# Kernel tuning notes

Hardware: AMD Instinct MI355X
Metric: run time of the kernel (lower is better)

Reference implementation:

```python
import jax, jax.numpy as jnp
import numpy as np

H = 16  # num heads
D = 64  # head dim


def rotate_half(x):
    h = x.shape[-1] // 2
    return jnp.concatenate([-x[..., h:], x[..., :h]], axis=-1)


def setup_inputs() -> dict:
    key = jax.random.key(0)
    ks = jax.random.split(key, 8)
    B, S, E = 2, 4096, 1024
    scale = 1.0 / np.sqrt(E)
    x = jax.random.normal(ks[0], (B, S, E), dtype=jnp.float32)
    Wq = jax.random.normal(ks[1], (E, E), dtype=jnp.float32) * scale
    Wk = jax.random.normal(ks[2], (E, E), dtype=jnp.float32) * scale
    Wv = jax.random.normal(ks[3], (E, E), dtype=jnp.float32) * scale
    Wg = jax.random.normal(ks[4], (E, E), dtype=jnp.float32) * scale
    Wo = jax.random.normal(ks[5], (E, E), dtype=jnp.float32) * scale
    cos = jax.random.normal(ks[6], (S, D), dtype=jnp.float32)
    sin = jax.random.normal(ks[7], (S, D), dtype=jnp.float32)
    return {"x": x, "Wq": Wq, "Wk": Wk, "Wv": Wv, "Wg": Wg, "Wo": Wo,
            "cos": cos, "sin": sin, "block_size": 256}


def reference(x, Wq, Wk, Wv, Wg, Wo, cos, sin, block_size):
    B, S, E = x.shape
    nb = S // block_size  # seq divisible by block_size (remainder==0 path)

    gate = (x @ Wg).reshape(B, S, H, D)
    q = (x @ Wq).reshape(B, S, H, D)
    k = (x @ Wk).reshape(B, S, H, D)
    v = (x @ Wv).reshape(B, S, H, D)

    # RoPE: cos/sin [S, D] -> broadcast over batch and heads (unsqueeze_dim=1 in torch
    # with [S, 1, D] after slicing gives the same broadcast over the head axis here).
    c = cos[:S][None, :, None, :]  # [1, S, 1, D]
    s = sin[:S][None, :, None, :]
    q = q * c + rotate_half(q) * s
    k = k * c + rotate_half(k) * s

    # Block-diagonal attention: reshape seq into blocks and attend within blocks only.
    def to_blocks(t):  # [B,S,H,D] -> [B,nb,H,block,D]
        return t.reshape(B, nb, block_size, H, D).transpose(0, 1, 3, 2, 4)

    qb, kb, vb = to_blocks(q), to_blocks(k), to_blocks(v)
    scores = jnp.einsum('bnhqd,bnhkd->bnhqk', qb, kb) / np.sqrt(D)
    attn = jax.nn.softmax(scores, axis=-1)
    ob = jnp.einsum('bnhqk,bnhkd->bnhqd', attn, vb)

    out = ob.transpose(0, 1, 3, 2, 4).reshape(B, S, H, D)  # back to [B,S,H,D]
    out = (out * jax.nn.sigmoid(gate)).reshape(B, S, H * D)
    return out @ Wo
```

## Files before the change

### kernel.cpp

```cpp
#include <hip/hip_runtime.h>
#include <hip/hip_bf16.h>
#include <stdint.h>

typedef __bf16 bf16_t;
typedef __bf16 bf16x8 __attribute__((ext_vector_type(8)));
typedef float f32x4 __attribute__((ext_vector_type(4)));

#define DEVI __device__ __forceinline__

constexpr int BB = 2;
constexpr int SS = 4096;
constexpr int EE = 1024;
constexpr int HH = 16;
constexpr int DD = 64;
constexpr int MM = BB * SS;

DEVI void gload16(const void* g, void* l) {
  __builtin_amdgcn_global_load_lds(
      (const __attribute__((address_space(1))) void*)g,
      (__attribute__((address_space(3))) void*)l, 16, 0, 0);
}

__global__ void cvt_kernel(const float* __restrict__ in, bf16_t* __restrict__ out, int n8) {
  int i = blockIdx.x * 256 + threadIdx.x;
  if (i >= n8) return;
  const float* p = in + (size_t)i * 8;
  bf16x8 o;
#pragma unroll
  for (int j = 0; j < 8; ++j) o[j] = (bf16_t)p[j];
  *(bf16x8*)(out + (size_t)i * 8) = o;
}

__global__ void wt_kernel(const float* __restrict__ w0, const float* __restrict__ w1,
                          const float* __restrict__ w2, const float* __restrict__ w3,
                          const float* __restrict__ w4, bf16_t* __restrict__ out) {
  __shared__ float tile[32][33];
  const float* Wsel = blockIdx.z == 0 ? w0 : blockIdx.z == 1 ? w1 :
                      blockIdx.z == 2 ? w2 : blockIdx.z == 3 ? w3 : w4;
  bf16_t* O = out + (size_t)blockIdx.z * EE * EE;
  int n0 = blockIdx.x * 32, k0 = blockIdx.y * 32;
  int tx = threadIdx.x & 31, ty = threadIdx.x >> 5;
#pragma unroll
  for (int i = 0; i < 4; ++i)
    tile[ty + i * 8][tx] = Wsel[(size_t)(k0 + ty + i * 8) * EE + n0 + tx];
  __syncthreads();
#pragma unroll
  for (int i = 0; i < 4; ++i)
    O[(size_t)(n0 + ty + i * 8) * EE + k0 + tx] = (bf16_t)tile[tx][ty + i * 8];
}

__global__ __launch_bounds__(512, 2) void gemm8p(const bf16_t* __restrict__ A,
                                                 const bf16_t* __restrict__ Bt,
                                                 bf16_t* __restrict__ Obase,
                                                 const float* __restrict__ cosp,
                                                 const float* __restrict__ sinp) {
  __shared__ bf16_t Al[2][2][128][64];
  __shared__ bf16_t Bl[2][2][128][64];
  const int id = blockIdx.x;
  const int swz = (id & 7) * 64 + (id >> 3);
  const int bx = swz >> 4, by = swz & 15;
  const int m0 = bx << 8, n0 = by << 8;
  const int tid = threadIdx.x, wv = tid >> 6, ln = tid & 63;
  const int wm = wv >> 2, wn = wv & 3;
  const int sr = tid >> 3;
  const int scs = (tid & 7) ^ (sr & 7);
  const bf16_t* Abase = A + ((size_t)(m0 + sr) << 10) + scs * 8;
  const bf16_t* Bbase = Bt + ((size_t)(n0 + sr) << 10) + scs * 8;

  f32x4 acc[8][4] = {};
  bf16x8 bfr[4][2];

#define STA(BUFI, H, J, KT) \
  gload16(Abase + (((H)*128 + (J)*64) << 10) + (KT)*64, &Al[BUFI][H][(J)*64 + wv * 8][0])
#define STB(BUFI, H, J, KT) \
  gload16(Bbase + (((H)*128 + (J)*64) << 10) + (KT)*64, &Bl[BUFI][H][(J)*64 + wv * 8][0])
#define STB_ALL(BUFI, KT) do { STB(BUFI,0,0,KT); STB(BUFI,0,1,KT); STB(BUFI,1,0,KT); STB(BUFI,1,1,KT); } while (0)

#define PHASE(BUFI, MH, KK, LDB, STAGEC, WAITC) do {                           \
    bf16x8 af_[4];                                                             \
    _Pragma("unroll") for (int mi_ = 0; mi_ < 4; ++mi_) {                      \
      int ar_ = (MH)*64 + mi_*16 + (ln & 15);                                  \
      int ach_ = ((KK)*4 + (ln >> 4)) ^ (ar_ & 7);                             \
      af_[mi_] = *(const bf16x8*)&Al[BUFI][wm][ar_][ach_ * 8];                 \
    }                                                                          \
    if (LDB) {                                                                 \
      _Pragma("unroll") for (int ni_ = 0; ni_ < 4; ++ni_) {                    \
        int br_ = (wn & 1)*64 + ni_*16 + (ln & 15);                            \
        int bch_ = ((KK)*4 + (ln >> 4)) ^ (br_ & 7);                           \
        bfr[ni_][KK] = *(const bf16x8*)&Bl[BUFI][wn >> 1][br_][bch_ * 8];      \
      }                                                                        \
    }                                                                          \
    STAGEC;                                                                    \
    WAITC;                                                                     \
    __builtin_amdgcn_s_barrier();                                              \
    asm volatile("s_waitcnt lgkmcnt(0)" ::: "memory");                         \
    __builtin_amdgcn_sched_barrier(0);                                         \
    __builtin_amdgcn_s_setprio(1);                                             \
    _Pragma("unroll") for (int mi_ = 0; mi_ < 4; ++mi_)                        \
      _Pragma("unroll") for (int ni_ = 0; ni_ < 4; ++ni_)                      \
        acc[(MH)*4 + mi_][ni_] = __builtin_amdgcn_mfma_f32_16x16x32_bf16(      \
            af_[mi_], bfr[ni_][KK], acc[(MH)*4 + mi_][ni_], 0, 0, 0);          \
    __builtin_amdgcn_s_setprio(0);                                             \
    __builtin_amdgcn_s_barrier();                                              \
    asm volatile("" ::: "memory");                                             \
  } while (0)

  STA(0, 0, 0, 0); STA(0, 1, 0, 0);
  STB_ALL(0, 0);
  STA(0, 0, 1, 0); STA(0, 1, 1, 0);
  STA(1, 0, 0, 1); STA(1, 1, 0, 1);
  STB_ALL(1, 1);
  asm volatile("s_waitcnt vmcnt(6)" ::: "memory");
  __builtin_amdgcn_s_barrier();
  asm volatile("" ::: "memory");

#pragma unroll 1
  for (int i = 0; i < 7; ++i) {
    const int to = 2 * i + 1;
    PHASE(0, 0, 0, 1, ({ STA(1, 0, 1, to); STA(1, 1, 1, to); }), ((void)0));
    PHASE(0, 0, 1, 1, ((void)0), ((void)0));
    PHASE(0, 1, 0, 0, ({ STA(0, 0, 0, to + 1); STA(0, 1, 0, to + 1); STB_ALL(0, to + 1); }),
          ((void)0));
    PHASE(0, 1, 1, 0, ((void)0), ({ asm volatile("s_waitcnt vmcnt(6)" ::: "memory"); }));
    PHASE(1, 0, 0, 1, ({ STA(0, 0, 1, to + 1); STA(0, 1, 1, to + 1); }), ((void)0));
    PHASE(1, 0, 1, 1, ((void)0), ((void)0));
    PHASE(1, 1, 0, 0, ({ STA(1, 0, 0, to + 2); STA(1, 1, 0, to + 2); STB_ALL(1, to + 2); }),
          ((void)0));
    PHASE(1, 1, 1, 0, ((void)0), ({ asm volatile("s_waitcnt vmcnt(6)" ::: "memory"); }));
  }
  PHASE(0, 0, 0, 1, ({ STA(1, 0, 1, 15); STA(1, 1, 1, 15); }), ((void)0));
  PHASE(0, 0, 1, 1, ((void)0), ((void)0));
  PHASE(0, 1, 0, 0, ((void)0), ((void)0));
  PHASE(0, 1, 1, 0, ((void)0), ({ asm volatile("s_waitcnt vmcnt(0)" ::: "memory"); }));
  PHASE(1, 0, 0, 1, ((void)0), ((void)0));
  PHASE(1, 0, 1, 1, ((void)0), ((void)0));
  PHASE(1, 1, 0, 0, ((void)0), ((void)0));
  PHASE(1, 1, 1, 0, ((void)0), ((void)0));
#undef PHASE
#undef STA
#undef STB
#undef STB_ALL

  const int widx = n0 >> 10;
  const int cb = (n0 & 1023) + wn * 64;
  bf16_t* W = Obase + (size_t)widx * MM * EE;
  if (widx <= 1) {
#pragma unroll
    for (int mi = 0; mi < 8; ++mi) {
#pragma unroll
      for (int r = 0; r < 4; ++r) {
        int row = m0 + wm * 128 + mi * 16 + ((ln >> 4) << 2) + r;
        int s = row & (SS - 1);
        float cv[4], sv[4];
#pragma unroll
        for (int ni = 0; ni < 4; ++ni) {
          int d = ni * 16 + (ln & 15);
          cv[ni] = cosp[s * DD + d];
          sv[ni] = sinp[s * DD + d];
        }
#pragma unroll
        for (int ni = 0; ni < 4; ++ni) {
          float v = acc[mi][ni][r], p = acc[mi][ni ^ 2][r];
          float o = v * cv[ni] + (ni < 2 ? -p : p) * sv[ni];
          W[(size_t)row * EE + cb + ni * 16 + (ln & 15)] = (bf16_t)o;
        }
      }
    }
  } else if (widx == 2) {
#pragma unroll
    for (int mi = 0; mi < 8; ++mi)
#pragma unroll
      for (int ni = 0; ni < 4; ++ni) {
        int row = m0 + wm * 128 + mi * 16 + ((ln >> 4) << 2);
        int ncol = cb + ni * 16 + (ln & 15);
        int h = ncol >> 6, d = ncol & 63;
        int b = row >> 12, s = row & (SS - 1);
        bf16_t* p = W + (((size_t)b * HH + h) * DD + d) * SS + s;
#pragma unroll
        for (int r = 0; r < 4; ++r) p[r] = (bf16_t)acc[mi][ni][r];
      }
  } else {
#pragma unroll
    for (int mi = 0; mi < 8; ++mi)
#pragma unroll
      for (int ni = 0; ni < 4; ++ni) {
        int row = m0 + wm * 128 + mi * 16 + ((ln >> 4) << 2);
        int ncol = cb + ni * 16 + (ln & 15);
        bf16_t* p = W + (size_t)row * EE + ncol;
#pragma unroll
        for (int r = 0; r < 4; ++r) p[(size_t)r * EE] = (bf16_t)acc[mi][ni][r];
      }
  }
}

__global__ __launch_bounds__(256) void gemm_out(const bf16_t* __restrict__ A,
                                                const bf16_t* __restrict__ Bt,
                                                float* __restrict__ O) {
  __shared__ bf16_t Al[128 * 64];
  __shared__ bf16_t Bl[128 * 64];
  const int m0 = blockIdx.x * 128;
  const int n0 = blockIdx.y * 128;
  const int tid = threadIdx.x;
  const int wv = tid >> 6, ln = tid & 63;
  const int wm = wv >> 1, wn = wv & 1;
  f32x4 acc[4][4] = {};

  for (int k0 = 0; k0 < EE; k0 += 64) {
    __syncthreads();
#pragma unroll
    for (int i = 0; i < 4; ++i) {
      int slot = i * 256 + wv * 64 + ln;
      int r = slot >> 3, c = slot & 7;
      int cs = c ^ (r & 7);
      gload16(A + (size_t)(m0 + r) * EE + k0 + cs * 8, Al + (size_t)(i * 256 + wv * 64) * 8);
      gload16(Bt + (size_t)(n0 + r) * EE + k0 + cs * 8, Bl + (size_t)(i * 256 + wv * 64) * 8);
    }
    __syncthreads();
#pragma unroll
    for (int kk = 0; kk < 2; ++kk) {
      bf16x8 af[4], bfr[4];
#pragma unroll
      for (int mi = 0; mi < 4; ++mi) {
        int row = wm * 64 + mi * 16 + (ln & 15);
        int ch = (kk * 4 + (ln >> 4)) ^ (row & 7);
        af[mi] = *(const bf16x8*)(Al + row * 64 + ch * 8);
      }
#pragma unroll
      for (int ni = 0; ni < 4; ++ni) {
        int row = wn * 64 + ni * 16 + (ln & 15);
        int ch = (kk * 4 + (ln >> 4)) ^ (row & 7);
        bfr[ni] = *(const bf16x8*)(Bl + row * 64 + ch * 8);
      }
#pragma unroll
      for (int mi = 0; mi < 4; ++mi)
#pragma unroll
        for (int ni = 0; ni < 4; ++ni)
          acc[mi][ni] = __builtin_amdgcn_mfma_f32_16x16x32_bf16(af[mi], bfr[ni], acc[mi][ni], 0, 0, 0);
    }
  }

#pragma unroll
  for (int mi = 0; mi < 4; ++mi)
#pragma unroll
    for (int ni = 0; ni < 4; ++ni) {
      int row = m0 + wm * 64 + mi * 16 + ((ln >> 4) << 2);
      int col = n0 + wn * 64 + ni * 16 + (ln & 15);
#pragma unroll
      for (int r = 0; r < 4; ++r) O[(size_t)(row + r) * EE + col] = acc[mi][ni][r];
    }
}

__global__ __launch_bounds__(256) void attn_kernel(const bf16_t* __restrict__ Q,
                                                   const bf16_t* __restrict__ Kc,
                                                   const bf16_t* __restrict__ Vt,
                                                   const bf16_t* __restrict__ G,
                                                   bf16_t* __restrict__ AO) {
  __shared__ bf16_t Kl[2][64 * 64];
  __shared__ bf16_t Vl[2][64 * 64];
  __shared__ bf16_t Pl[4][64 * 64];
  const int bx = blockIdx.x;
  const int h = bx & 15, sb = (bx >> 4) & 15, b = bx >> 8;
  const int tid = threadIdx.x, wv = tid >> 6, ln = tid & 63;
  const int qrow0 = b * SS + sb * 256 + wv * 64;

  bf16x8 qf[4][2];
#pragma unroll
  for (int mi = 0; mi < 4; ++mi)
#pragma unroll
    for (int kk = 0; kk < 2; ++kk)
      qf[mi][kk] = *(const bf16x8*)(Q + (size_t)(qrow0 + mi * 16 + (ln & 15)) * EE +
                                    h * DD + kk * 32 + ((ln >> 4) << 3));

  f32x4 o[4][4] = {};
  float mr[4][4], lr[4][4];
#pragma unroll
  for (int i = 0; i < 4; ++i)
#pragma unroll
    for (int r = 0; r < 4; ++r) { mr[i][r] = -1e30f; lr[i][r] = 0.f; }

#define STAGE_KV(KC, BI) do {                                                        \
    const int krow0_ = b * SS + sb * 256 + (KC) * 64;                                \
    _Pragma("unroll") for (int i_ = 0; i_ < 2; ++i_) {                               \
      int slot_ = i_ * 256 + wv * 64 + ln;                                           \
      int r_ = slot_ >> 3, c_ = slot_ & 7, cs_ = c_ ^ (r_ & 7);                      \
      gload16(Kc + (size_t)(krow0_ + r_) * EE + h * DD + cs_ * 8,                    \
              &Kl[BI][(i_ * 256 + wv * 64) * 8]);                                    \
      gload16(Vt + (((size_t)b * HH + h) * DD + r_) * SS + sb * 256 + (KC) * 64 +    \
                  cs_ * 8,                                                           \
              &Vl[BI][(i_ * 256 + wv * 64) * 8]);                                    \
    }                                                                                \
  } while (0)

  STAGE_KV(0, 0);
  __syncthreads();

  for (int kc = 0; kc < 4; ++kc) {
    const int cur = kc & 1;
    if (kc < 3) STAGE_KV(kc + 1, cur ^ 1);

    f32x4 sc[4][4] = {};
    __builtin_amdgcn_s_setprio(1);
#pragma unroll
    for (int kk = 0; kk < 2; ++kk) {
      bf16x8 kf[4];
#pragma unroll
      for (int ni = 0; ni < 4; ++ni) {
        int row = ni * 16 + (ln & 15);
        int ch = (kk * 4 + (ln >> 4)) ^ (row & 7);
        kf[ni] = *(const bf16x8*)(&Kl[cur][row * 64 + ch * 8]);
      }
#pragma unroll
      for (int mi = 0; mi < 4; ++mi)
#pragma unroll
        for (int ni = 0; ni < 4; ++ni)
          sc[mi][ni] = __builtin_amdgcn_mfma_f32_16x16x32_bf16(qf[mi][kk], kf[ni], sc[mi][ni], 0, 0, 0);
    }
    __builtin_amdgcn_s_setprio(0);
#pragma unroll
    for (int mi = 0; mi < 4; ++mi)
#pragma unroll
      for (int ni = 0; ni < 4; ++ni) sc[mi][ni] *= 0.125f;

#pragma unroll
    for (int mi = 0; mi < 4; ++mi) {
#pragma unroll
      for (int r = 0; r < 4; ++r) {
        float mx = fmaxf(fmaxf(sc[mi][0][r], sc[mi][1][r]), fmaxf(sc[mi][2][r], sc[mi][3][r]));
#pragma unroll
        for (int d = 1; d < 16; d <<= 1) mx = fmaxf(mx, __shfl_xor(mx, d));
        float mn = fmaxf(mr[mi][r], mx);
        float scal = __expf(mr[mi][r] - mn);
        mr[mi][r] = mn;
        float rs = 0.f;
#pragma unroll
        for (int ni = 0; ni < 4; ++ni) {
          float p = __expf(sc[mi][ni][r] - mn);
          sc[mi][ni][r] = p;
          rs += p;
        }
#pragma unroll
        for (int d = 1; d < 16; d <<= 1) rs += __shfl_xor(rs, d);
        lr[mi][r] = lr[mi][r] * scal + rs;
#pragma unroll
        for (int nd = 0; nd < 4; ++nd) o[mi][nd][r] *= scal;
      }
    }

    bf16_t* P = Pl[wv];
#pragma unroll
    for (int mi = 0; mi < 4; ++mi)
#pragma unroll
      for (int ni = 0; ni < 4; ++ni)
#pragma unroll
        for (int r = 0; r < 4; ++r) {
          int row = mi * 16 + ((ln >> 4) << 2) + r;
          int col = ni * 16 + (ln & 15);
          P[row * 64 + (col ^ ((row & 7) << 3))] = (bf16_t)sc[mi][ni][r];
        }
    __builtin_amdgcn_s_setprio(1);
#pragma unroll
    for (int kk = 0; kk < 2; ++kk) {
      bf16x8 pf[4], vf[4];
#pragma unroll
      for (int mi = 0; mi < 4; ++mi) {
        int row = mi * 16 + (ln & 15);
        int ch = (kk * 4 + (ln >> 4)) ^ (row & 7);
        pf[mi] = *(const bf16x8*)(P + row * 64 + ch * 8);
      }
#pragma unroll
      for (int nd = 0; nd < 4; ++nd) {
        int row = nd * 16 + (ln & 15);
        int ch = (kk * 4 + (ln >> 4)) ^ (row & 7);
        vf[nd] = *(const bf16x8*)(&Vl[cur][row * 64 + ch * 8]);
      }
#pragma unroll
      for (int mi = 0; mi < 4; ++mi)
#pragma unroll
        for (int nd = 0; nd < 4; ++nd)
          o[mi][nd] = __builtin_amdgcn_mfma_f32_16x16x32_bf16(pf[mi], vf[nd], o[mi][nd], 0, 0, 0);
    }
    __builtin_amdgcn_s_setprio(0);
    __syncthreads();
  }
#undef STAGE_KV

#pragma unroll
  for (int mi = 0; mi < 4; ++mi)
#pragma unroll
    for (int nd = 0; nd < 4; ++nd)
#pragma unroll
      for (int r = 0; r < 4; ++r) {
        int m = qrow0 + mi * 16 + ((ln >> 4) << 2) + r;
        int col = h * DD + nd * 16 + (ln & 15);
        float gv = (float)G[(size_t)m * EE + col];
        float sig = 1.f / (1.f + __expf(-gv));
        AO[(size_t)m * EE + col] = (bf16_t)((o[mi][nd][r] / lr[mi][r]) * sig);
      }
}

extern "C" void kernel_launch(void* const* d_in, const int* in_sizes, int n_in,
                              void* d_out, int out_size, void* d_ws, size_t ws_size,
                              hipStream_t stream) {
  const float* x = (const float*)d_in[0];
  const float* Wq = (const float*)d_in[1];
  const float* Wk = (const float*)d_in[2];
  const float* Wv = (const float*)d_in[3];
  const float* Wg = (const float*)d_in[4];
  const float* Wo = (const float*)d_in[5];
  const float* cosp = (const float*)d_in[6];
  const float* sinp = (const float*)d_in[7];
  float* out = (float*)d_out;

  char* ws = (char*)d_ws;
  bf16_t* XB = (bf16_t*)(ws);
  bf16_t* WT = (bf16_t*)(ws + (16ll << 20));
  bf16_t* QB = (bf16_t*)(ws + (26ll << 20));
  bf16_t* KB = (bf16_t*)(ws + (42ll << 20));
  bf16_t* VT = (bf16_t*)(ws + (58ll << 20));
  bf16_t* GB = (bf16_t*)(ws + (74ll << 20));
  bf16_t* AO = XB;

  const int n8 = MM * EE / 8;
  cvt_kernel<<<n8 / 256, 256, 0, stream>>>(x, XB, n8);
  wt_kernel<<<dim3(32, 32, 5), 256, 0, stream>>>(Wq, Wk, Wv, Wg, Wo, WT);
  gemm8p<<<512, 512, 0, stream>>>(XB, WT, QB, cosp, sinp);
  attn_kernel<<<BB * (SS / 256) * HH, 256, 0, stream>>>(QB, KB, VT, GB, AO);
  gemm_out<<<dim3(MM / 128, EE / 128), 256, 0, stream>>>(AO, WT + (size_t)4 * EE * EE, out);
}
```

Baseline: 178.8 us.

## Restructure GEMM global-to-LDS prefetch schedule and drop sched_barrier

Reorders the 256x256 GEMM main loop so the A and B tile loads into LDS are spread evenly across the eight MFMA phases, two loads per phase. The loop now runs eight iterations with guarded loads instead of seven plus a peeled epilogue, and the vmcnt waits change from 6 to 4. The aim is smoother memory issue and better overlap of loads with MFMAs. It also removes the sched_barrier before the MFMA block, which lets the compiler move instructions across that point but risks it undoing the hand-written interleaving.

```diff
diff --git a/kernel.cpp b/kernel.cpp
--- a/kernel.cpp
+++ b/kernel.cpp
@@ -74,7 +74,6 @@
   gload16(Abase + (((H)*128 + (J)*64) << 10) + (KT)*64, &Al[BUFI][H][(J)*64 + wv * 8][0])
 #define STB(BUFI, H, J, KT) \
   gload16(Bbase + (((H)*128 + (J)*64) << 10) + (KT)*64, &Bl[BUFI][H][(J)*64 + wv * 8][0])
-#define STB_ALL(BUFI, KT) do { STB(BUFI,0,0,KT); STB(BUFI,0,1,KT); STB(BUFI,1,0,KT); STB(BUFI,1,1,KT); } while (0)
 
 #define PHASE(BUFI, MH, KK, LDB, STAGEC, WAITC) do {                           \
     bf16x8 af_[4];                                                             \
@@ -94,7 +93,6 @@
     WAITC;                                                                     \
     __builtin_amdgcn_s_barrier();                                              \
     asm volatile("s_waitcnt lgkmcnt(0)" ::: "memory");                         \
-    __builtin_amdgcn_sched_barrier(0);                                         \
     __builtin_amdgcn_s_setprio(1);                                             \
     _Pragma("unroll") for (int mi_ = 0; mi_ < 4; ++mi_)                        \
       _Pragma("unroll") for (int ni_ = 0; ni_ < 4; ++ni_)                      \
@@ -105,41 +103,35 @@
     asm volatile("" ::: "memory");                                             \
   } while (0)
 
-  STA(0, 0, 0, 0); STA(0, 1, 0, 0);
-  STB_ALL(0, 0);
-  STA(0, 0, 1, 0); STA(0, 1, 1, 0);
-  STA(1, 0, 0, 1); STA(1, 1, 0, 1);
-  STB_ALL(1, 1);
-  asm volatile("s_waitcnt vmcnt(6)" ::: "memory");
+  STA(0, 0, 0, 0); STA(0, 0, 1, 0); STA(0, 1, 0, 0); STA(0, 1, 1, 0);
+  STB(0, 0, 0, 0); STB(0, 0, 1, 0); STB(0, 1, 0, 0); STB(0, 1, 1, 0);
+  STB(1, 0, 0, 1); STB(1, 0, 1, 1); STB(1, 1, 0, 1); STB(1, 1, 1, 1);
+  asm volatile("s_waitcnt vmcnt(4)" ::: "memory");
   __builtin_amdgcn_s_barrier();
   asm volatile("" ::: "memory");
 
 #pragma unroll 1
-  for (int i = 0; i < 7; ++i) {
+  for (int i = 0; i < 8; ++i) {
     const int to = 2 * i + 1;
-    PHASE(0, 0, 0, 1, ({ STA(1, 0, 1, to); STA(1, 1, 1, to); }), ((void)0));
-    PHASE(0, 0, 1, 1, ((void)0), ((void)0));
-    PHASE(0, 1, 0, 0, ({ STA(0, 0, 0, to + 1); STA(0, 1, 0, to + 1); STB_ALL(0, to + 1); }),
+    PHASE(0, 0, 0, 1, ({ STA(1, 0, 0, to); STA(1, 0, 1, to); }), ((void)0));
+    PHASE(0, 0, 1, 1, ({ STA(1, 1, 0, to); STA(1, 1, 1, to); }), ((void)0));
+    PHASE(0, 1, 0, 0, ({ if (i < 7) { STB(0, 0, 0, to + 1); STB(0, 0, 1, to + 1); } }),
           ((void)0));
-    PHASE(0, 1, 1, 0, ((void)0), ({ asm volatile("s_waitcnt vmcnt(6)" ::: "memory"); }));
-    PHASE(1, 0, 0, 1, ({ STA(0, 0, 1, to + 1); STA(0, 1, 1, to + 1); }), ((void)0));
-    PHASE(1, 0, 1, 1, ((void)0), ((void)0));
-    PHASE(1, 1, 0, 0, ({ STA(1, 0, 0, to + 2); STA(1, 1, 0, to + 2); STB_ALL(1, to + 2); }),
+    PHASE(0, 1, 1, 0, ({ if (i < 7) { STB(0, 1, 0, to + 1); STB(0, 1, 1, to + 1); } }),
+          ({ if (i < 7) { asm volatile("s_waitcnt vmcnt(4)" ::: "memory"); }
+             else       { asm volatile("s_waitcnt vmcnt(0)" ::: "memory"); } }));
+    PHASE(1, 0, 0, 1, ({ if (i < 7) { STA(0, 0, 0, to + 1); STA(0, 0, 1, to + 1); } }),
           ((void)0));
-    PHASE(1, 1, 1, 0, ((void)0), ({ asm volatile("s_waitcnt vmcnt(6)" ::: "memory"); }));
+    PHASE(1, 0, 1, 1, ({ if (i < 7) { STA(0, 1, 0, to + 1); STA(0, 1, 1, to + 1); } }),
+          ((void)0));
+    PHASE(1, 1, 0, 0, ({ if (i < 7) { STB(1, 0, 0, to + 2); STB(1, 0, 1, to + 2); } }),
+          ((void)0));
+    PHASE(1, 1, 1, 0, ({ if (i < 7) { STB(1, 1, 0, to + 2); STB(1, 1, 1, to + 2); } }),
+          ({ if (i < 7) { asm volatile("s_waitcnt vmcnt(4)" ::: "memory"); } }));
   }
-  PHASE(0, 0, 0, 1, ({ STA(1, 0, 1, 15); STA(1, 1, 1, 15); }), ((void)0));
-  PHASE(0, 0, 1, 1, ((void)0), ((void)0));
-  PHASE(0, 1, 0, 0, ((void)0), ((void)0));
-  PHASE(0, 1, 1, 0, ((void)0), ({ asm volatile("s_waitcnt vmcnt(0)" ::: "memory"); }));
-  PHASE(1, 0, 0, 1, ((void)0), ((void)0));
-  PHASE(1, 0, 1, 1, ((void)0), ((void)0));
-  PHASE(1, 1, 0, 0, ((void)0), ((void)0));
-  PHASE(1, 1, 1, 0, ((void)0), ((void)0));
 #undef PHASE
 #undef STA
 #undef STB
-#undef STB_ALL
 
   const int widx = n0 >> 10;
   const int cb = (n0 & 1023) + wn * 64;
```

New measurement: 177.1 us. About the same (-1.0%).
